# Performance work log

Hardware: AMD Instinct MI355X
Metric: run time of the kernel (lower is better)

The kernel has to match this reference:

```python
import jax, jax.numpy as jnp
import numpy as np

NUM_EMBEDDINGS = 1024
EMBEDDING_DIM = 64
COMMITMENT_COST = 0.25


def setup_inputs() -> dict:
    key = jax.random.key(0)
    k1, k2 = jax.random.split(key)
    z_e = jax.random.normal(k1, (32, EMBEDDING_DIM, 32, 32), dtype=jnp.float32)
    # codebook init: uniform(-1/K, 1/K) as in the torch module
    embedding = jax.random.uniform(
        k2, (NUM_EMBEDDINGS, EMBEDDING_DIM), dtype=jnp.float32,
        minval=-1.0 / NUM_EMBEDDINGS, maxval=1.0 / NUM_EMBEDDINGS)
    return {"z_e": z_e, "embedding": embedding}


def reference(z_e, embedding):
    B, C, H, W = z_e.shape
    # (B,C,H,W) -> (B,H,W,C) -> (N,C)
    z = jnp.transpose(z_e, (0, 2, 3, 1))
    z_flat = z.reshape(-1, C)
    # squared L2 distances: |z|^2 - 2 z e^T + |e|^2  -> (N, K)
    distances = (jnp.sum(z_flat ** 2, axis=1, keepdims=True)
                 - 2.0 * z_flat @ embedding.T
                 + jnp.sum(embedding ** 2, axis=1))
    encoding_indices = jnp.argmin(distances, axis=1)  # (N,)
    z_q = embedding[encoding_indices].reshape(z.shape)  # (B,H,W,C)
    # use_ema=True branch: loss = commitment_cost * mse(z, sg(z_q))
    commitment_loss = jnp.mean((z - jax.lax.stop_gradient(z_q)) ** 2)
    loss = COMMITMENT_COST * commitment_loss
    # straight-through estimator
    z_q_ste = z + jax.lax.stop_gradient(z_q - z)
    z_q_ste = jnp.transpose(z_q_ste, (0, 3, 1, 2))  # back to (B,C,H,W)
    indices = encoding_indices.reshape(B, H, W)
    return z_q_ste, loss, indices
```

## Files before the change

kernel.cpp:

```cpp
#include <hip/hip_runtime.h>
#include <hip/hip_bf16.h>
#include <math.h>
#include <stdint.h>

#define NUM_EMB 1024
#define DIM 64
#define LOSS_OFF 2097152
#define IDX_OFF 2097153
#define NROWS 32768
#define CAND_CAP 1024

typedef float f32x4 __attribute__((ext_vector_type(4)));
typedef short bf16x8 __attribute__((ext_vector_type(8)));

__device__ __forceinline__ float np_fold16(float* y) {
#pragma unroll
    for (int j = 0; j < 8; ++j) y[j] = __fadd_rn(y[j], y[j + 8]);
#pragma unroll
    for (int j = 0; j < 4; ++j) y[j] = __fadd_rn(y[j], y[j + 4]);
    y[0] = __fadd_rn(y[0], y[2]);
    y[1] = __fadd_rn(y[1], y[3]);
    return __fadd_rn(y[0], y[1]);
}

__device__ __forceinline__ unsigned short bf16bits(float f) {
    __hip_bfloat16 h = __float2bfloat16(f);
    return *reinterpret_cast<unsigned short*>(&h);
}

__global__ void vq_emb_norms(const float* __restrict__ emb,
                             float* __restrict__ norms,
                             float* __restrict__ out) {
    int k = blockIdx.x * blockDim.x + threadIdx.x;
    if (k == 0) out[LOSS_OFF] = 0.0f;
    if (k < NUM_EMB) {
        const float4* e4 = reinterpret_cast<const float4*>(emb + k * DIM);
        float e2[DIM];
#pragma unroll
        for (int q = 0; q < 16; ++q) {
            const float4 v = e4[q];
            e2[q * 4 + 0] = v.x; e2[q * 4 + 1] = v.y;
            e2[q * 4 + 2] = v.z; e2[q * 4 + 3] = v.w;
        }
        float y[16];
#pragma unroll
        for (int j = 0; j < 16; ++j) {
            float a = __fadd_rn(__fmul_rn(e2[j],      e2[j]),
                                __fmul_rn(e2[j + 16], e2[j + 16]));
            float b = __fadd_rn(__fmul_rn(e2[j + 32], e2[j + 32]),
                                __fmul_rn(e2[j + 48], e2[j + 48]));
            y[j] = __fadd_rn(a, b);
        }
        norms[k] = np_fold16(y);
    }
}

__device__ inline unsigned long long exact_key(
        const float* __restrict__ z_e, const float* __restrict__ emb,
        const float* __restrict__ norms, long zrowbase, int k) {
    float z[DIM];
#pragma unroll
    for (int c = 0; c < DIM; ++c) z[c] = z_e[zrowbase + (long)c * 1024];
    float A;
    {
        float y[16];
#pragma unroll
        for (int j = 0; j < 16; ++j) {
            float a  = __fadd_rn(__fmul_rn(z[j],      z[j]),
                                 __fmul_rn(z[j + 16], z[j + 16]));
            float c2 = __fadd_rn(__fmul_rn(z[j + 32], z[j + 32]),
                                 __fmul_rn(z[j + 48], z[j + 48]));
            y[j] = __fadd_rn(a, c2);
        }
        A = np_fold16(y);
    }
    const float4* ep = reinterpret_cast<const float4*>(emb + (size_t)k * DIM);
    float dot = 0.f;
#pragma unroll
    for (int q = 0; q < 16; ++q) {
        const float4 e4 = ep[q];
        dot = __fmaf_rn(z[4 * q + 0], e4.x, dot);
        dot = __fmaf_rn(z[4 * q + 1], e4.y, dot);
        dot = __fmaf_rn(z[4 * q + 2], e4.z, dot);
        dot = __fmaf_rn(z[4 * q + 3], e4.w, dot);
    }
    const float d = __fadd_rn(__fmaf_rn(-2.f, dot, A), norms[k]);
    return ((unsigned long long)__float_as_uint(d) << 32) | (unsigned)k;
}

__device__ __forceinline__ void stage_ebf(short* s_ebf,
                                          const float* __restrict__ emb,
                                          int ch, int tid) {
#pragma unroll
    for (int it = 0; it < 8; ++it) {
        const int idx = it * 512 + tid;
        const int cl  = idx >> 4;
        const int cq  = idx & 15;
        const float4 v = *reinterpret_cast<const float4*>(
            emb + (size_t)(ch * 256 + cl) * 64 + 4 * cq);
        uint2 pk;
        pk.x = (unsigned)bf16bits(v.x) | ((unsigned)bf16bits(v.y) << 16);
        pk.y = (unsigned)bf16bits(v.z) | ((unsigned)bf16bits(v.w) << 16);
        const int byte = cl * 128 + ((8 * cq) ^ ((cl & 7) << 4));
        *reinterpret_cast<uint2*>(reinterpret_cast<char*>(s_ebf) + byte) = pk;
    }
}

__device__ __forceinline__ f32x4 tile_dot(const short* s_ebf, int cl, int kb,
                                          bf16x8 a0, bf16x8 a1) {
    const char* base = reinterpret_cast<const char*>(s_ebf) + cl * 128;
    const int sw = (cl & 7) << 4;
    const bf16x8 b0 = *reinterpret_cast<const bf16x8*>(base + ((16 * kb) ^ sw));
    const bf16x8 b1 = *reinterpret_cast<const bf16x8*>(base + ((64 + 16 * kb) ^ sw));
    f32x4 C = {0.f, 0.f, 0.f, 0.f};
    C = __builtin_amdgcn_mfma_f32_16x16x32_bf16(a0, b0, C, 0, 0, 0);
    C = __builtin_amdgcn_mfma_f32_16x16x32_bf16(a1, b1, C, 0, 0, 0);
    return C;
}

__global__ __launch_bounds__(512, 4)
void vq_mfma_fused(const float* __restrict__ z_e,
                   const float* __restrict__ emb,
                   const float* __restrict__ norms,
                   float* __restrict__ out) {
    __shared__ short s_zbf[64 * 64];
    __shared__ short s_ebf[256 * 64];
    __shared__ float s_pmin[2][64];
    __shared__ float s_S[64];
    __shared__ unsigned int s_cand[CAND_CAP];
    __shared__ int s_cnt;
    __shared__ unsigned long long s_key[64];
    __shared__ int s_final[64];
    __shared__ float s_loss[8];

    const int tid  = threadIdx.x;
    const int lane = tid & 63;
    const int wave = __builtin_amdgcn_readfirstlane(tid >> 6);
    const int rt    = wave & 3;
    const int chalf = wave >> 2;

    const int n0  = blockIdx.x * 64;
    const int b   = n0 >> 10;
    const int hw0 = n0 & 1023;

    if (tid == 0) s_cnt = 0;
    if (tid < 64) s_key[tid] = ~0ull;

#pragma unroll
    for (int it = 0; it < 4; ++it) {
        const int idx = it * 512 + tid;
        const int hw  = idx & 63;
        const int cp  = idx >> 6;
        const float f0 = z_e[(long)b * 65536 + (long)(2 * cp)     * 1024 + hw0 + hw];
        const float f1 = z_e[(long)b * 65536 + (long)(2 * cp + 1) * 1024 + hw0 + hw];
        const unsigned int pk =
            (unsigned int)bf16bits(f0) | ((unsigned int)bf16bits(f1) << 16);
        const int byte = hw * 128 + ((4 * cp) ^ ((hw & 7) << 4));
        *reinterpret_cast<unsigned int*>(
            reinterpret_cast<char*>(s_zbf) + byte) = pk;
    }
    __syncthreads();

    const int rowA = rt * 16 + (lane & 15);
    const int kb   = lane >> 4;
    bf16x8 a0, a1;
    {
        const char* base = reinterpret_cast<const char*>(s_zbf) + rowA * 128;
        const int sw = (rowA & 7) << 4;
        a0 = *reinterpret_cast<const bf16x8*>(base + ((16 * kb) ^ sw));
        a1 = *reinterpret_cast<const bf16x8*>(base + ((64 + 16 * kb) ^ sw));
    }
    if (chalf == 0) {
        float s = 0.f;
#pragma unroll
        for (int j = 0; j < 8; ++j) {
            s += fabsf(__uint_as_float(((unsigned)(unsigned short)a0[j]) << 16));
            s += fabsf(__uint_as_float(((unsigned)(unsigned short)a1[j]) << 16));
        }
        s += __shfl_xor(s, 16, 64);
        s += __shfl_xor(s, 32, 64);
        if (kb == 0) s_S[rowA] = s;
    }

    float bestv[4] = {INFINITY, INFINITY, INFINITY, INFINITY};
    float secv[4]  = {INFINITY, INFINITY, INFINITY, INFINITY};
    int   bestc[4] = {0, 0, 0, 0};
    int   secc[4]  = {0, 0, 0, 0};

    for (int ch = 0; ch < 4; ++ch) {
        __syncthreads();
        stage_ebf(s_ebf, emb, ch, tid);
        __syncthreads();
#pragma unroll
        for (int tt = 0; tt < 8; ++tt) {
            const int t    = chalf * 8 + tt;
            const int cl   = t * 16 + (lane & 15);
            const int code = ch * 256 + cl;
            const f32x4 C  = tile_dot(s_ebf, cl, kb, a0, a1);
            const float Ek = norms[code];
#pragma unroll
            for (int r = 0; r < 4; ++r) {
                const float v = __fmaf_rn(-2.f, C[r], Ek);
                if (v < bestv[r]) {
                    secv[r] = bestv[r]; secc[r] = bestc[r];
                    bestv[r] = v;       bestc[r] = code;
                } else if (v < secv[r]) {
                    secv[r] = v;        secc[r] = code;
                }
            }
        }
    }

#pragma unroll
    for (int r = 0; r < 4; ++r) {
        float m = bestv[r];
        m = fminf(m, __shfl_xor(m, 1, 64));
        m = fminf(m, __shfl_xor(m, 2, 64));
        m = fminf(m, __shfl_xor(m, 4, 64));
        m = fminf(m, __shfl_xor(m, 8, 64));
        if ((lane & 15) == 0)
            s_pmin[chalf][rt * 16 + (lane >> 4) * 4 + r] = m;
    }
    __syncthreads();

#pragma unroll
    for (int r = 0; r < 4; ++r) {
        const int row = rt * 16 + (lane >> 4) * 4 + r;
        const float rowmin = fminf(s_pmin[0][row], s_pmin[1][row]);
        const float thr = rowmin + (3.0517578125e-5f * s_S[row] + 2e-4f);
        if (secv[r] <= thr) {
            for (int ch = 0; ch < 4; ++ch)
#pragma unroll
                for (int tt = 0; tt < 8; ++tt) {
                    const int code =
                        ch * 256 + (chalf * 8 + tt) * 16 + (lane & 15);
                    const int slot = atomicAdd(&s_cnt, 1);
                    if (slot < CAND_CAP)
                        s_cand[slot] = ((unsigned)row << 10) | (unsigned)code;
                }
        } else if (bestv[r] <= thr) {
            const int slot = atomicAdd(&s_cnt, 1);
            if (slot < CAND_CAP)
                s_cand[slot] = ((unsigned)row << 10) | (unsigned)bestc[r];
        }
    }
    __syncthreads();

    const int cnt = s_cnt;
    if (cnt <= CAND_CAP) {
        for (int i = tid; i < cnt; i += 512) {
            const unsigned int e = s_cand[i];
            const int row = (int)(e >> 10);
            const int k   = (int)(e & 1023u);
            const unsigned long long key =
                exact_key(z_e, emb, norms, (long)b * 65536 + hw0 + row, k);
            atomicMin(&s_key[row], key);
        }
    } else {
        for (int j = tid; j < 64 * 1024; j += 512) {
            const int row = j >> 10;
            const int k   = j & 1023;
            const unsigned long long key =
                exact_key(z_e, emb, norms, (long)b * 65536 + hw0 + row, k);
            atomicMin(&s_key[row], key);
        }
    }
    __syncthreads();

    if (tid < 64) {
        const int k = (int)(s_key[tid] & 0xFFFFFFFFull);
        s_final[tid] = k;
        out[IDX_OFF + n0 + tid] = (float)k;
    }
    __syncthreads();

    const long zbase = (long)b * 65536 + hw0 + lane;
    const int fidx = s_final[lane];
    float lsum = 0.f;
#pragma unroll
    for (int j = 0; j < DIM / 8; ++j) {
        const int c = wave * 8 + j;
        const float zc = z_e[zbase + (long)c * 1024];
        const float ec = emb[fidx * DIM + c];
        out[((long)(b * 64 + c)) * 1024 + hw0 + lane] = zc + (ec - zc);
        const float dlt = zc - ec;
        lsum = __fmaf_rn(dlt, dlt, lsum);
    }
#pragma unroll
    for (int off = 32; off >= 1; off >>= 1) lsum += __shfl_xor(lsum, off, 64);
    if (lane == 0) s_loss[wave] = lsum;
    __syncthreads();

    if (tid == 0) {
        float t = 0.f;
#pragma unroll
        for (int w = 0; w < 8; ++w) t = __fadd_rn(t, s_loss[w]);
        atomicAdd(out + LOSS_OFF, t * 1.1920928955078125e-07f);
    }
}

extern "C" void kernel_launch(void* const* d_in, const int* in_sizes, int n_in,
                              void* d_out, int out_size, void* d_ws, size_t ws_size,
                              hipStream_t stream) {
    const float* z_e = (const float*)d_in[0];
    const float* emb = (const float*)d_in[1];
    float* out   = (float*)d_out;
    float* norms = (float*)d_ws;

    vq_emb_norms<<<dim3(16), dim3(64), 0, stream>>>(emb, norms, out);
    vq_mfma_fused<<<dim3(NROWS / 64), dim3(512), 0, stream>>>(z_e, emb, norms, out);
}
```

Before: 101.0 us.

## Prefetch codebook chunks into registers and compute norms per block

Codebook norms are no longer computed in a separate kernel. Each block now computes all 1024 norms into shared memory, so the 64-thread norm kernel is replaced by a trivial loss-zeroing launch. Codebook chunks are register-prefetched one chunk ahead, so the global loads for the next chunk overlap the MFMA scan of the current one, and one barrier per chunk is dropped. The cost is redundant norm computation (every block reads the full 256KB codebook) plus extra registers and 4KB more shared memory per block, which may lower occupancy.

Result: slower. 111.3 us (+10.1%).

```diff
diff --git a/kernel.cpp b/kernel.cpp
--- a/kernel.cpp
+++ b/kernel.cpp
@@ -28,36 +28,13 @@
     return *reinterpret_cast<unsigned short*>(&h);
 }
 
-__global__ void vq_emb_norms(const float* __restrict__ emb,
-                             float* __restrict__ norms,
-                             float* __restrict__ out) {
-    int k = blockIdx.x * blockDim.x + threadIdx.x;
-    if (k == 0) out[LOSS_OFF] = 0.0f;
-    if (k < NUM_EMB) {
-        const float4* e4 = reinterpret_cast<const float4*>(emb + k * DIM);
-        float e2[DIM];
-#pragma unroll
-        for (int q = 0; q < 16; ++q) {
-            const float4 v = e4[q];
-            e2[q * 4 + 0] = v.x; e2[q * 4 + 1] = v.y;
-            e2[q * 4 + 2] = v.z; e2[q * 4 + 3] = v.w;
-        }
-        float y[16];
-#pragma unroll
-        for (int j = 0; j < 16; ++j) {
-            float a = __fadd_rn(__fmul_rn(e2[j],      e2[j]),
-                                __fmul_rn(e2[j + 16], e2[j + 16]));
-            float b = __fadd_rn(__fmul_rn(e2[j + 32], e2[j + 32]),
-                                __fmul_rn(e2[j + 48], e2[j + 48]));
-            y[j] = __fadd_rn(a, b);
-        }
-        norms[k] = np_fold16(y);
-    }
+__global__ void vq_zero(float* __restrict__ out) {
+    if (threadIdx.x == 0) out[LOSS_OFF] = 0.0f;
 }
 
 __device__ inline unsigned long long exact_key(
         const float* __restrict__ z_e, const float* __restrict__ emb,
-        const float* __restrict__ norms, long zrowbase, int k) {
+        const float* norms, long zrowbase, int k) {
     float z[DIM];
 #pragma unroll
     for (int c = 0; c < DIM; ++c) z[c] = z_e[zrowbase + (long)c * 1024];
@@ -86,24 +63,6 @@
     }
     const float d = __fadd_rn(__fmaf_rn(-2.f, dot, A), norms[k]);
     return ((unsigned long long)__float_as_uint(d) << 32) | (unsigned)k;
-}
-
-__device__ __forceinline__ void stage_ebf(short* s_ebf,
-                                          const float* __restrict__ emb,
-                                          int ch, int tid) {
-#pragma unroll
-    for (int it = 0; it < 8; ++it) {
-        const int idx = it * 512 + tid;
-        const int cl  = idx >> 4;
-        const int cq  = idx & 15;
-        const float4 v = *reinterpret_cast<const float4*>(
-            emb + (size_t)(ch * 256 + cl) * 64 + 4 * cq);
-        uint2 pk;
-        pk.x = (unsigned)bf16bits(v.x) | ((unsigned)bf16bits(v.y) << 16);
-        pk.y = (unsigned)bf16bits(v.z) | ((unsigned)bf16bits(v.w) << 16);
-        const int byte = cl * 128 + ((8 * cq) ^ ((cl & 7) << 4));
-        *reinterpret_cast<uint2*>(reinterpret_cast<char*>(s_ebf) + byte) = pk;
-    }
 }
 
 __device__ __forceinline__ f32x4 tile_dot(const short* s_ebf, int cl, int kb,
@@ -121,10 +80,10 @@
 __global__ __launch_bounds__(512, 4)
 void vq_mfma_fused(const float* __restrict__ z_e,
                    const float* __restrict__ emb,
-                   const float* __restrict__ norms,
                    float* __restrict__ out) {
     __shared__ short s_zbf[64 * 64];
     __shared__ short s_ebf[256 * 64];
+    __shared__ float s_norm[NUM_EMB];
     __shared__ float s_pmin[2][64];
     __shared__ float s_S[64];
     __shared__ unsigned int s_cand[CAND_CAP];
@@ -145,6 +104,14 @@
 
     if (tid == 0) s_cnt = 0;
     if (tid < 64) s_key[tid] = ~0ull;
+
+    const float4* emb4 = reinterpret_cast<const float4*>(emb);
+    float4 pf[8];
+#pragma unroll
+    for (int it = 0; it < 8; ++it) {
+        const int idx = it * 512 + tid;
+        pf[it] = emb4[(size_t)(idx >> 4) * 16 + (idx & 15)];
+    }
 
 #pragma unroll
     for (int it = 0; it < 4; ++it) {
@@ -159,6 +126,29 @@
         *reinterpret_cast<unsigned int*>(
             reinterpret_cast<char*>(s_zbf) + byte) = pk;
     }
+
+#pragma unroll
+    for (int kk = 0; kk < 2; ++kk) {
+        const int k = kk * 512 + tid;
+        const float4* e4 = reinterpret_cast<const float4*>(emb + (size_t)k * DIM);
+        float e2[DIM];
+#pragma unroll
+        for (int q = 0; q < 16; ++q) {
+            const float4 v = e4[q];
+            e2[q * 4 + 0] = v.x; e2[q * 4 + 1] = v.y;
+            e2[q * 4 + 2] = v.z; e2[q * 4 + 3] = v.w;
+        }
+        float y[16];
+#pragma unroll
+        for (int j = 0; j < 16; ++j) {
+            float a = __fadd_rn(__fmul_rn(e2[j],      e2[j]),
+                                __fmul_rn(e2[j + 16], e2[j + 16]));
+            float bb = __fadd_rn(__fmul_rn(e2[j + 32], e2[j + 32]),
+                                 __fmul_rn(e2[j + 48], e2[j + 48]));
+            y[j] = __fadd_rn(a, bb);
+        }
+        s_norm[k] = np_fold16(y);
+    }
     __syncthreads();
 
     const int rowA = rt * 16 + (lane & 15);
@@ -182,32 +172,72 @@
         if (kb == 0) s_S[rowA] = s;
     }
 
+#pragma unroll
+    for (int it = 0; it < 8; ++it) {
+        const int idx = it * 512 + tid;
+        const int cl  = idx >> 4;
+        const int cq  = idx & 15;
+        uint2 pk;
+        pk.x = (unsigned)bf16bits(pf[it].x) | ((unsigned)bf16bits(pf[it].y) << 16);
+        pk.y = (unsigned)bf16bits(pf[it].z) | ((unsigned)bf16bits(pf[it].w) << 16);
+        const int byte = cl * 128 + ((8 * cq) ^ ((cl & 7) << 4));
+        *reinterpret_cast<uint2*>(reinterpret_cast<char*>(s_ebf) + byte) = pk;
+    }
+#pragma unroll
+    for (int it = 0; it < 8; ++it) {
+        const int idx = it * 512 + tid;
+        pf[it] = emb4[(size_t)(256 + (idx >> 4)) * 16 + (idx & 15)];
+    }
+    __syncthreads();
+
     float bestv[4] = {INFINITY, INFINITY, INFINITY, INFINITY};
     float secv[4]  = {INFINITY, INFINITY, INFINITY, INFINITY};
     int   bestc[4] = {0, 0, 0, 0};
-    int   secc[4]  = {0, 0, 0, 0};
 
     for (int ch = 0; ch < 4; ++ch) {
-        __syncthreads();
-        stage_ebf(s_ebf, emb, ch, tid);
-        __syncthreads();
 #pragma unroll
         for (int tt = 0; tt < 8; ++tt) {
             const int t    = chalf * 8 + tt;
             const int cl   = t * 16 + (lane & 15);
             const int code = ch * 256 + cl;
             const f32x4 C  = tile_dot(s_ebf, cl, kb, a0, a1);
-            const float Ek = norms[code];
+            const float Ek = s_norm[code];
 #pragma unroll
             for (int r = 0; r < 4; ++r) {
                 const float v = __fmaf_rn(-2.f, C[r], Ek);
                 if (v < bestv[r]) {
-                    secv[r] = bestv[r]; secc[r] = bestc[r];
-                    bestv[r] = v;       bestc[r] = code;
+                    secv[r]  = bestv[r];
+                    bestv[r] = v;  bestc[r] = code;
                 } else if (v < secv[r]) {
-                    secv[r] = v;        secc[r] = code;
+                    secv[r] = v;
                 }
             }
+        }
+        if (ch < 3) {
+            __syncthreads();
+#pragma unroll
+            for (int it = 0; it < 8; ++it) {
+                const int idx = it * 512 + tid;
+                const int cl  = idx >> 4;
+                const int cq  = idx & 15;
+                uint2 pk;
+                pk.x = (unsigned)bf16bits(pf[it].x) |
+                       ((unsigned)bf16bits(pf[it].y) << 16);
+                pk.y = (unsigned)bf16bits(pf[it].z) |
+                       ((unsigned)bf16bits(pf[it].w) << 16);
+                const int byte = cl * 128 + ((8 * cq) ^ ((cl & 7) << 4));
+                *reinterpret_cast<uint2*>(
+                    reinterpret_cast<char*>(s_ebf) + byte) = pk;
+            }
+            if (ch < 2) {
+#pragma unroll
+                for (int it = 0; it < 8; ++it) {
+                    const int idx = it * 512 + tid;
+                    pf[it] = emb4[(size_t)((ch + 2) * 256 + (idx >> 4)) * 16 +
+                                  (idx & 15)];
+                }
+            }
+            __syncthreads();
         }
     }
 
@@ -253,7 +283,7 @@
             const int row = (int)(e >> 10);
             const int k   = (int)(e & 1023u);
             const unsigned long long key =
-                exact_key(z_e, emb, norms, (long)b * 65536 + hw0 + row, k);
+                exact_key(z_e, emb, s_norm, (long)b * 65536 + hw0 + row, k);
             atomicMin(&s_key[row], key);
         }
     } else {
@@ -261,7 +291,7 @@
             const int row = j >> 10;
             const int k   = j & 1023;
             const unsigned long long key =
-                exact_key(z_e, emb, norms, (long)b * 65536 + hw0 + row, k);
+                exact_key(z_e, emb, s_norm, (long)b * 65536 + hw0 + row, k);
             atomicMin(&s_key[row], key);
         }
     }
@@ -304,9 +334,9 @@
                               hipStream_t stream) {
     const float* z_e = (const float*)d_in[0];
     const float* emb = (const float*)d_in[1];
-    float* out   = (float*)d_out;
-    float* norms = (float*)d_ws;
-
-    vq_emb_norms<<<dim3(16), dim3(64), 0, stream>>>(emb, norms, out);
-    vq_mfma_fused<<<dim3(NROWS / 64), dim3(512), 0, stream>>>(z_e, emb, norms, out);
-}
+    float* out = (float*)d_out;
+    (void)d_ws; (void)ws_size;
+
+    vq_zero<<<dim3(1), dim3(64), 0, stream>>>(out);
+    vq_mfma_fused<<<dim3(NROWS / 64), dim3(512), 0, stream>>>(z_e, emb, out);
+}
```
